# Kernel optimization log

Measured on AMD Instinct MI355X. Metric: run time of the kernel, lower is better.

Reference implementation:

```python
import jax, jax.numpy as jnp
import numpy as np

D_MODEL = 1024
NUM_HEADS = 16
D_K = D_MODEL // NUM_HEADS
EPS = 1e-6


def setup_inputs() -> dict:
    key = jax.random.key(0)
    ks = jax.random.split(key, 16)
    B, S = 2, 2048
    sc_in = 1.0 / np.sqrt(D_MODEL)
    sc_na = 1.0 / np.sqrt(D_K)
    inp = {
        "Q": jax.random.normal(ks[0], (B, S, D_MODEL), jnp.float32),
        "K": jax.random.normal(ks[1], (B, S, D_MODEL), jnp.float32),
        "V": jax.random.normal(ks[2], (B, S, D_MODEL), jnp.float32),
        "mask": jax.random.randint(ks[3], (1, 1, S, S), 0, 2, jnp.int32),
        # projection weights stored [in, out] (math-equivalent to torch Linear)
        "wq": jax.random.normal(ks[4], (D_MODEL, D_MODEL), jnp.float32) * sc_in,
        "bq": jnp.zeros((D_MODEL,), jnp.float32),
        "wk": jax.random.normal(ks[5], (D_MODEL, D_MODEL), jnp.float32) * sc_in,
        "bk": jnp.zeros((D_MODEL,), jnp.float32),
        "wv": jax.random.normal(ks[6], (D_MODEL, D_MODEL), jnp.float32) * sc_in,
        "bv": jnp.zeros((D_MODEL,), jnp.float32),
        "wo": jax.random.normal(ks[7], (D_MODEL, D_MODEL), jnp.float32) * sc_in,
        "bo": jnp.zeros((D_MODEL,), jnp.float32),
        # NeuralAttention score-fn params (per-head-dim transforms)
        "wnq": jax.random.normal(ks[8], (D_K, D_K), jnp.float32) * sc_na,
        "bnq": jnp.zeros((D_K,), jnp.float32),
        "wnk": jax.random.normal(ks[9], (D_K, D_K), jnp.float32) * sc_na,
        "bnk": jnp.zeros((D_K,), jnp.float32),
        "temperature": jnp.ones((NUM_HEADS, 1, 1), jnp.float32),
        "gamma": jnp.ones((D_MODEL,), jnp.float32),
    }
    return inp


def _split_heads(x):
    B, S, _ = x.shape
    return x.reshape(B, S, NUM_HEADS, D_K).transpose(0, 2, 1, 3)  # [B,H,S,dk]


def reference(Q, K, V, mask, wq, bq, wk, bk, wv, bv, wo, bo,
              wnq, bnq, wnk, bnk, temperature, gamma):
    B, S, _ = Q.shape
    q = _split_heads(Q @ wq + bq)  # [B,H,S,dk]
    k = _split_heads(K @ wk + bk)
    v = _split_heads(V @ wv + bv)
    # NeuralAttention: nonlinear per-token feature maps, then contraction
    qf = jnp.tanh(q @ wnq + bnq)
    kf = jnp.tanh(k @ wnk + bnk)
    scores = jnp.einsum('bhqd,bhkd->bhqk', qf, kf) / jnp.sqrt(jnp.float32(D_K))
    scores = scores / temperature  # [H,1,1] broadcasts over [B,H,S,S]
    scores = jnp.where(mask == 0, jnp.float32(-1e9), scores)
    attn = jax.nn.softmax(scores, axis=-1)
    ctx = jnp.einsum('bhqk,bhkd->bhqd', attn, v)
    out = ctx.transpose(0, 2, 1, 3).reshape(B, S, D_MODEL) @ wo + bo
    # RMSNorm
    rms = jax.lax.rsqrt(jnp.mean(out * out, axis=-1, keepdims=True) + EPS)
    return out * rms * gamma
```

## Files before the change

kernel.cpp:

```cpp
#include <hip/hip_runtime.h>
#include <hip/hip_bf16.h>
#include <math.h>

#define S_LEN 2048
#define BATCH 2
#define NH 16
#define DK 64
#define DM 1024
#define BS (BATCH * S_LEN)
#define BHS (BATCH * NH * S_LEN)

using bf16x8  = __attribute__((ext_vector_type(8))) __bf16;
using floatx4 = __attribute__((ext_vector_type(4))) float;
using ushort8v = __attribute__((ext_vector_type(8))) unsigned short;
using ushort4v = __attribute__((ext_vector_type(4))) unsigned short;

__device__ __forceinline__ unsigned short f2bf(float f) {
    union { float f; unsigned u; } v; v.f = f;
    unsigned r = v.u + 0x7fffu + ((v.u >> 16) & 1u);
    return (unsigned short)(r >> 16);
}

__device__ __forceinline__ void gl2lds16(const void* g, void* l) {
    __builtin_amdgcn_global_load_lds(
        (__attribute__((address_space(1))) void*)(uintptr_t)g,
        (__attribute__((address_space(3))) void*)(uintptr_t)l,
        16, 0, 0);
}

__global__ void k_convert(const float* __restrict__ q, const float* __restrict__ k,
                          const float* __restrict__ v,
                          unsigned short* __restrict__ qb, unsigned short* __restrict__ kb,
                          unsigned short* __restrict__ vb) {
    const int N4 = BS * DM / 4;
    int i = blockIdx.x * 256 + threadIdx.x;
    int which = i / N4;
    int off = i - which * N4;
    const floatx4* src = (const floatx4*)(which == 0 ? q : which == 1 ? k : v);
    unsigned short* dst = which == 0 ? qb : which == 1 ? kb : vb;
    floatx4 x = src[off];
    ushort4v o;
    o[0] = f2bf(x[0]); o[1] = f2bf(x[1]); o[2] = f2bf(x[2]); o[3] = f2bf(x[3]);
    ((ushort4v*)dst)[off] = o;
}

__global__ void k_transpose(const float* s0, const float* s1, const float* s2, const float* s3,
                            unsigned short* d0, unsigned short* d1, unsigned short* d2,
                            unsigned short* d3, int n) {
    int z = blockIdx.z;
    const float* src = z == 0 ? s0 : z == 1 ? s1 : z == 2 ? s2 : s3;
    unsigned short* dst = z == 0 ? d0 : z == 1 ? d1 : z == 2 ? d2 : d3;
    __shared__ unsigned short tile[32][33];
    int tx = threadIdx.x & 31, ty = threadIdx.x >> 5;
#pragma unroll
    for (int i = 0; i < 4; i++) {
        int y = blockIdx.y * 32 + i * 8 + ty;
        tile[i * 8 + ty][tx] = f2bf(src[(size_t)y * n + blockIdx.x * 32 + tx]);
    }
    __syncthreads();
#pragma unroll
    for (int i = 0; i < 4; i++) {
        int r = blockIdx.x * 32 + i * 8 + ty;
        dst[(size_t)r * n + blockIdx.y * 32 + tx] = tile[tx][i * 8 + ty];
    }
}

__global__ void k_maskpack(const int* __restrict__ mask, unsigned int* __restrict__ mb) {
    int t = blockIdx.x * 256 + threadIdx.x;
    int row = t >> 6, w = t & 63;
    const int* p = mask + (size_t)row * S_LEN + w * 32;
    unsigned bits = 0;
#pragma unroll
    for (int i = 0; i < 32; i++) bits |= (p[i] != 0 ? 1u : 0u) << i;
    mb[t] = bits;
}

__global__ __launch_bounds__(256) void k_gemm_qkv(
    const unsigned short* __restrict__ Qb, const unsigned short* __restrict__ Kb,
    const unsigned short* __restrict__ Vb,
    const unsigned short* __restrict__ Wqt, const unsigned short* __restrict__ Wkt,
    const unsigned short* __restrict__ Wvt,
    const float* __restrict__ bq, const float* __restrict__ bk, const float* __restrict__ bv,
    unsigned short* __restrict__ qh, unsigned short* __restrict__ kh,
    unsigned short* __restrict__ vfrag) {
    const int K = DM;
    int z = blockIdx.z;
    const unsigned short* A  = z == 0 ? Qb  : z == 1 ? Kb  : Vb;
    const unsigned short* Wt = z == 0 ? Wqt : z == 1 ? Wkt : Wvt;
    const float* bias        = z == 0 ? bq  : z == 1 ? bk  : bv;
    int m0 = blockIdx.y * 128, n0 = blockIdx.x * 128;
    __shared__ unsigned short As[128 * 32];
    __shared__ unsigned short Bs[128 * 32];
    int tid = threadIdx.x;
    int lane = tid & 63, wid = tid >> 6;
    int wy = wid >> 1, wx = wid & 1;
    int l16 = lane & 15, quad = lane >> 4;

    floatx4 acc[4][4] = {};

    for (int kt = 0; kt < K / 32; kt++) {
        int kk = kt * 32;
#pragma unroll
        for (int i = 0; i < 2; i++) {
            int c = i * 256 + tid;
            int row = c >> 2, seg = c & 3;
            gl2lds16(A + (size_t)(m0 + row) * K + kk + seg * 8, &As[c * 8]);
            gl2lds16(Wt + (size_t)(n0 + row) * K + kk + seg * 8, &Bs[c * 8]);
        }
        __syncthreads();
        bf16x8 af[4], bf[4];
#pragma unroll
        for (int mi = 0; mi < 4; mi++)
            af[mi] = *(const bf16x8*)&As[(wy * 64 + mi * 16 + l16) * 32 + quad * 8];
#pragma unroll
        for (int ni = 0; ni < 4; ni++)
            bf[ni] = *(const bf16x8*)&Bs[(wx * 64 + ni * 16 + l16) * 32 + quad * 8];
#pragma unroll
        for (int mi = 0; mi < 4; mi++)
#pragma unroll
            for (int ni = 0; ni < 4; ni++)
                acc[mi][ni] = __builtin_amdgcn_mfma_f32_16x16x32_bf16(af[mi], bf[ni], acc[mi][ni], 0, 0, 0);
        __syncthreads();
    }

#pragma unroll
    for (int mi = 0; mi < 4; mi++) {
#pragma unroll
        for (int ni = 0; ni < 4; ni++) {
            int col = n0 + wx * 64 + ni * 16 + l16;
            float bvv = bias[col];
            int row = m0 + wy * 64 + mi * 16 + quad * 4;
            int b = row >> 11;
            int head = col >> 6;
            int d = col & 63;
            if (z < 2) {
                unsigned short* out = z == 0 ? qh : kh;
                int s = row & (S_LEN - 1);
#pragma unroll
                for (int r = 0; r < 4; r++)
                    out[(size_t)((b * NH + head) * S_LEN + s + r) * DK + d] =
                        f2bf(acc[mi][ni][r] + bvv);
            } else {
                int bh = b * NH + head;
                int kt2 = (row & (S_LEN - 1)) >> 6;
                int ks = mi >> 1;
                int qf = (mi * 2 + (quad >> 1)) & 3;
                int j0 = (quad & 1) * 4;
                size_t off = ((size_t)bh * 32 + kt2) * 4096 +
                             (size_t)(((d >> 4) * 2 + ks) * 512 + (qf * 16 + (d & 15)) * 8 + j0);
                ushort4v o;
#pragma unroll
                for (int r = 0; r < 4; r++) o[r] = f2bf(acc[mi][ni][r] + bvv);
                *(ushort4v*)&vfrag[off] = o;
            }
        }
    }
}

__global__ __launch_bounds__(256) void k_gemm_out(const unsigned short* __restrict__ A,
                                                  const unsigned short* __restrict__ Wt,
                                                  const float* __restrict__ bias,
                                                  float* __restrict__ out_f32) {
    const int K = DM;
    int m0 = blockIdx.y * 128, n0 = blockIdx.x * 128;
    __shared__ unsigned short As[128 * 32];
    __shared__ unsigned short Bs[128 * 32];
    int tid = threadIdx.x;
    int lane = tid & 63, wid = tid >> 6;
    int wy = wid >> 1, wx = wid & 1;
    int l16 = lane & 15, quad = lane >> 4;

    floatx4 acc[4][4] = {};

    for (int kt = 0; kt < K / 32; kt++) {
        int kk = kt * 32;
#pragma unroll
        for (int i = 0; i < 2; i++) {
            int c = i * 256 + tid;
            int row = c >> 2, seg = c & 3;
            gl2lds16(A + (size_t)(m0 + row) * K + kk + seg * 8, &As[c * 8]);
            gl2lds16(Wt + (size_t)(n0 + row) * K + kk + seg * 8, &Bs[c * 8]);
        }
        __syncthreads();
        bf16x8 af[4], bf[4];
#pragma unroll
        for (int mi = 0; mi < 4; mi++)
            af[mi] = *(const bf16x8*)&As[(wy * 64 + mi * 16 + l16) * 32 + quad * 8];
#pragma unroll
        for (int ni = 0; ni < 4; ni++)
            bf[ni] = *(const bf16x8*)&Bs[(wx * 64 + ni * 16 + l16) * 32 + quad * 8];
#pragma unroll
        for (int mi = 0; mi < 4; mi++)
#pragma unroll
            for (int ni = 0; ni < 4; ni++)
                acc[mi][ni] = __builtin_amdgcn_mfma_f32_16x16x32_bf16(af[mi], bf[ni], acc[mi][ni], 0, 0, 0);
        __syncthreads();
    }

#pragma unroll
    for (int mi = 0; mi < 4; mi++) {
#pragma unroll
        for (int ni = 0; ni < 4; ni++) {
            int col = n0 + wx * 64 + ni * 16 + l16;
            float bvv = bias[col];
#pragma unroll
            for (int r = 0; r < 4; r++) {
                int row = m0 + wy * 64 + mi * 16 + quad * 4 + r;
                out_f32[(size_t)row * DM + col] = acc[mi][ni][r] + bvv;
            }
        }
    }
}

__global__ __launch_bounds__(256) void k_feature(const unsigned short* __restrict__ qh,
                                                 const unsigned short* __restrict__ kh,
                                                 const unsigned short* __restrict__ wnqt,
                                                 const unsigned short* __restrict__ wnkt,
                                                 const float* __restrict__ bnq,
                                                 const float* __restrict__ bnk,
                                                 unsigned short* __restrict__ qfb,
                                                 unsigned short* __restrict__ kfrag) {
    int zy = blockIdx.y;
    const unsigned short* src = zy == 0 ? qh : kh;
    const unsigned short* wt = zy == 0 ? wnqt : wnkt;
    const float* bias = zy == 0 ? bnq : bnk;

    int tid = threadIdx.x, lane = tid & 63, wid = tid >> 6;
    int l16 = lane & 15, quad = lane >> 4;
    int r0 = blockIdx.x * 64 + wid * 16;

    bf16x8 af[2];
#pragma unroll
    for (int ks = 0; ks < 2; ks++)
        af[ks] = *(const bf16x8*)(src + (size_t)(r0 + l16) * DK + ks * 32 + quad * 8);

    floatx4 acc[4] = {};
#pragma unroll
    for (int ni = 0; ni < 4; ni++) {
#pragma unroll
        for (int ks = 0; ks < 2; ks++) {
            bf16x8 bf = *(const bf16x8*)(wt + (size_t)(ni * 16 + l16) * DK + ks * 32 + quad * 8);
            acc[ni] = __builtin_amdgcn_mfma_f32_16x16x32_bf16(af[ks], bf, acc[ni], 0, 0, 0);
        }
    }
    if (zy == 0) {
#pragma unroll
        for (int ni = 0; ni < 4; ni++) {
            int col = ni * 16 + l16;
            float bv = bias[col];
#pragma unroll
            for (int r = 0; r < 4; r++) {
                float t = tanhf(acc[ni][r] + bv);
                qfb[(size_t)(r0 + quad * 4 + r) * DK + col] = f2bf(t);
            }
        }
    } else {
        int bh = r0 >> 11;
        int kt = (r0 & (S_LEN - 1)) >> 6;
        size_t base = ((size_t)bh * 32 + kt) * 4096;
#pragma unroll
        for (int ni = 0; ni < 4; ni++) {
            int col = ni * 16 + l16;
            float bv = bias[col];
            int ks = ni >> 1;
            int qf = (ni * 2 + (l16 >> 3)) & 3;
            int j = l16 & 7;
            size_t fo = base + (size_t)((wid * 2 + ks) * 512 + qf * 128 + j);
#pragma unroll
            for (int r = 0; r < 4; r++) {
                float t = tanhf(acc[ni][r] + bv);
                kfrag[fo + (quad * 4 + r) * 8] = f2bf(t);
            }
        }
    }
}

#define PSTR 72
__global__ __launch_bounds__(256, 4) void k_attn(const unsigned short* __restrict__ qf,
                                                 const unsigned short* __restrict__ kfr,
                                                 const unsigned short* __restrict__ vfr,
                                                 const unsigned long long* __restrict__ mb64,
                                                 const float* __restrict__ temp,
                                                 unsigned short* __restrict__ ctx) {
    int tid = threadIdx.x, lane = tid & 63, wid = tid >> 6;
    int l16 = lane & 15, quad = lane >> 4;
    int bh = blockIdx.y;
    int b = bh >> 4, h = bh & 15;
    int q0 = blockIdx.x * 64 + wid * 16;

    const unsigned short* qfb = qf + (size_t)bh * S_LEN * DK;
    const unsigned short* kbase = kfr + (size_t)bh * 32 * 4096;
    const unsigned short* vbase = vfr + (size_t)bh * 32 * 4096;
    float scale = 1.0f / (8.0f * temp[h]);

    __shared__ unsigned short Kbuf[2][4096];
    __shared__ unsigned short Plds[4][16 * PSTR];
    unsigned short* myP = Plds[wid];

    bf16x8 aq[2];
#pragma unroll
    for (int ks = 0; ks < 2; ks++)
        aq[ks] = *(const bf16x8*)(qfb + (size_t)(q0 + l16) * DK + ks * 32 + quad * 8);

    gl2lds16(kbase + tid * 8, &Kbuf[0][tid * 8]);
    gl2lds16(kbase + 2048 + tid * 8, &Kbuf[0][2048 + tid * 8]);

    floatx4 oacc[4] = {};
    float l_part[4] = {0.f, 0.f, 0.f, 0.f};
    int qrow = q0 + quad * 4;

    for (int kt = 0; kt < S_LEN / 64; kt++) {
        __syncthreads();
        int nb = (kt + 1) & 1;
        const unsigned short* kn = kbase + (size_t)((kt + 1) & 31) * 4096;
        gl2lds16(kn + tid * 8, &Kbuf[nb][tid * 8]);
        gl2lds16(kn + 2048 + tid * 8, &Kbuf[nb][2048 + tid * 8]);
        const unsigned short* vt = vbase + (size_t)kt * 4096 + lane * 8;
        bf16x8 vf[8];
#pragma unroll
        for (int i = 0; i < 8; i++) vf[i] = *(const bf16x8*)(vt + i * 512);
        unsigned long long mrow[4];
#pragma unroll
        for (int r = 0; r < 4; r++) mrow[r] = mb64[(size_t)(qrow + r) * 32 + kt];
        const unsigned short* kb = &Kbuf[kt & 1][lane * 8];
        bf16x8 kf8[8];
#pragma unroll
        for (int i = 0; i < 8; i++) kf8[i] = *(const bf16x8*)(kb + i * 512);
        floatx4 sf[4];
#pragma unroll
        for (int ni = 0; ni < 4; ni++) {
            floatx4 z = {};
            z = __builtin_amdgcn_mfma_f32_16x16x32_bf16(aq[0], kf8[ni * 2], z, 0, 0, 0);
            z = __builtin_amdgcn_mfma_f32_16x16x32_bf16(aq[1], kf8[ni * 2 + 1], z, 0, 0, 0);
            sf[ni] = z;
        }
#pragma unroll
        for (int ni = 0; ni < 4; ni++)
#pragma unroll
            for (int r = 0; r < 4; r++) {
                float s = ((mrow[r] >> (ni * 16 + l16)) & 1ull) ? sf[ni][r] * scale : -1e9f;
                float p = __expf(s);
                l_part[r] += p;
                myP[(quad * 4 + r) * PSTR + ni * 16 + l16] = f2bf(p);
            }
        bf16x8 pa[2];
#pragma unroll
        for (int ks = 0; ks < 2; ks++)
            pa[ks] = *(const bf16x8*)&myP[l16 * PSTR + ks * 32 + quad * 8];
#pragma unroll
        for (int ni = 0; ni < 4; ni++) {
            oacc[ni] = __builtin_amdgcn_mfma_f32_16x16x32_bf16(pa[0], vf[ni * 2], oacc[ni], 0, 0, 0);
            oacc[ni] = __builtin_amdgcn_mfma_f32_16x16x32_bf16(pa[1], vf[ni * 2 + 1], oacc[ni], 0, 0, 0);
        }
    }
#pragma unroll
    for (int r = 0; r < 4; r++) {
#pragma unroll
        for (int off = 1; off < 16; off <<= 1)
            l_part[r] += __shfl_xor(l_part[r], off, 16);
    }
    float inv[4];
#pragma unroll
    for (int r = 0; r < 4; r++) inv[r] = 1.0f / l_part[r];
#pragma unroll
    for (int ni = 0; ni < 4; ni++) {
        int d = ni * 16 + l16;
#pragma unroll
        for (int r = 0; r < 4; r++) {
            int s = q0 + quad * 4 + r;
            float val = oacc[ni][r] * inv[r];
            ctx[(size_t)(b * S_LEN + s) * DM + h * DK + d] = f2bf(val);
        }
    }
}

__global__ __launch_bounds__(256) void k_rmsnorm(const float* __restrict__ x,
                                                 const float* __restrict__ gamma,
                                                 float* __restrict__ out) {
    int row = blockIdx.x, tid = threadIdx.x;
    const floatx4* xr = (const floatx4*)(x + (size_t)row * DM);
    floatx4 v = xr[tid];
    float ss = v[0] * v[0] + v[1] * v[1] + v[2] * v[2] + v[3] * v[3];
#pragma unroll
    for (int off = 1; off < 64; off <<= 1) ss += __shfl_xor(ss, off);
    __shared__ float red[4];
    int lane = tid & 63, wid = tid >> 6;
    if (lane == 0) red[wid] = ss;
    __syncthreads();
    float tot = red[0] + red[1] + red[2] + red[3];
    float rms = rsqrtf(tot * (1.0f / DM) + 1e-6f);
    floatx4 g = ((const floatx4*)gamma)[tid];
    floatx4 o;
    o[0] = v[0] * rms * g[0];
    o[1] = v[1] * rms * g[1];
    o[2] = v[2] * rms * g[2];
    o[3] = v[3] * rms * g[3];
    ((floatx4*)(out + (size_t)row * DM))[tid] = o;
}

extern "C" void kernel_launch(void* const* d_in, const int* in_sizes, int n_in,
                              void* d_out, int out_size, void* d_ws, size_t ws_size,
                              hipStream_t stream) {
    const float* Q = (const float*)d_in[0];
    const float* K = (const float*)d_in[1];
    const float* V = (const float*)d_in[2];
    const int* mask = (const int*)d_in[3];
    const float* wq = (const float*)d_in[4];
    const float* bq = (const float*)d_in[5];
    const float* wk = (const float*)d_in[6];
    const float* bk = (const float*)d_in[7];
    const float* wv = (const float*)d_in[8];
    const float* bv = (const float*)d_in[9];
    const float* wo = (const float*)d_in[10];
    const float* bo = (const float*)d_in[11];
    const float* wnq = (const float*)d_in[12];
    const float* bnq = (const float*)d_in[13];
    const float* wnk = (const float*)d_in[14];
    const float* bnk = (const float*)d_in[15];
    const float* temp = (const float*)d_in[16];
    const float* gamma = (const float*)d_in[17];

    char* w = (char*)d_ws;
    size_t o = 0;
    auto alloc = [&](size_t bytes) {
        char* p = w + o;
        o += (bytes + 255) & ~(size_t)255;
        return p;
    };
    unsigned short* Qb = (unsigned short*)alloc((size_t)BS * DM * 2);
    unsigned short* Kb = (unsigned short*)alloc((size_t)BS * DM * 2);
    unsigned short* Vb = (unsigned short*)alloc((size_t)BS * DM * 2);
    unsigned short* Wqt = (unsigned short*)alloc((size_t)DM * DM * 2);
    unsigned short* Wkt = (unsigned short*)alloc((size_t)DM * DM * 2);
    unsigned short* Wvt = (unsigned short*)alloc((size_t)DM * DM * 2);
    unsigned short* Wot = (unsigned short*)alloc((size_t)DM * DM * 2);
    unsigned short* wnqt = (unsigned short*)alloc((size_t)DK * DK * 2);
    unsigned short* wnkt = (unsigned short*)alloc((size_t)DK * DK * 2);
    unsigned short* qh = (unsigned short*)alloc((size_t)BHS * DK * 2);
    unsigned short* kh = (unsigned short*)alloc((size_t)BHS * DK * 2);
    unsigned short* vfrag = (unsigned short*)alloc((size_t)BHS * DK * 2);
    unsigned short* qfb = (unsigned short*)alloc((size_t)BHS * DK * 2);
    unsigned short* kfrag = (unsigned short*)alloc((size_t)BHS * DK * 2);
    unsigned int* mb = (unsigned int*)alloc((size_t)S_LEN * (S_LEN / 32) * 4);
    unsigned short* ctx = (unsigned short*)alloc((size_t)BS * DM * 2);
    float* outt = (float*)alloc((size_t)BS * DM * 4);

    k_convert<<<dim3(3 * BS * DM / 4 / 256), 256, 0, stream>>>(Q, K, V, Qb, Kb, Vb);
    k_transpose<<<dim3(32, 32, 4), 256, 0, stream>>>(wq, wk, wv, wo, Wqt, Wkt, Wvt, Wot, DM);
    k_transpose<<<dim3(2, 2, 2), 256, 0, stream>>>(wnq, wnk, wnq, wnq, wnqt, wnkt, wnqt, wnqt, DK);
    k_maskpack<<<dim3(S_LEN * 64 / 256), 256, 0, stream>>>(mask, mb);

    k_gemm_qkv<<<dim3(8, 32, 3), 256, 0, stream>>>(Qb, Kb, Vb, Wqt, Wkt, Wvt,
                                                   bq, bk, bv, qh, kh, vfrag);

    k_feature<<<dim3(BHS / 64, 2), 256, 0, stream>>>(qh, kh, wnqt, wnkt, bnq, bnk, qfb, kfrag);

    k_attn<<<dim3(S_LEN / 64, BATCH * NH), 256, 0, stream>>>(
        qfb, kfrag, vfrag, (const unsigned long long*)mb, temp, ctx);

    k_gemm_out<<<dim3(8, 32), 256, 0, stream>>>(ctx, Wot, bo, outt);
    k_rmsnorm<<<dim3(BS), 256, 0, stream>>>(outt, gamma, (float*)d_out);
}
```

Baseline: 362.8 us.

## Stage epilogue stores through LDS, fold softmax scale into features, use exp2

Result: faster. 313.3 us (-13.6%).

```diff
diff --git a/kernel.cpp b/kernel.cpp
--- a/kernel.cpp
+++ b/kernel.cpp
@@ -9,16 +9,30 @@
 #define DM 1024
 #define BS (BATCH * S_LEN)
 #define BHS (BATCH * NH * S_LEN)
+#define TRP 72
+#define PSTR 72
 
 using bf16x8  = __attribute__((ext_vector_type(8))) __bf16;
 using floatx4 = __attribute__((ext_vector_type(4))) float;
-using ushort8v = __attribute__((ext_vector_type(8))) unsigned short;
 using ushort4v = __attribute__((ext_vector_type(4))) unsigned short;
+
+extern "C" __device__ float __ocml_exp2_f32(float);
 
 __device__ __forceinline__ unsigned short f2bf(float f) {
     union { float f; unsigned u; } v; v.f = f;
     unsigned r = v.u + 0x7fffu + ((v.u >> 16) & 1u);
     return (unsigned short)(r >> 16);
+}
+
+__device__ __forceinline__ unsigned cvt_pk_bf16(float a, float b) {
+    unsigned r;
+    asm("v_cvt_pk_bf16_f32 %0, %1, %2" : "=v"(r) : "v"(a), "v"(b));
+    return r;
+}
+
+__device__ __forceinline__ float fast_tanh(float x) {
+    float e = __ocml_exp2_f32(x * 2.8853900817779268f);
+    return 1.0f - 2.0f / (e + 1.0f);
 }
 
 __device__ __forceinline__ void gl2lds16(const void* g, void* l) {
@@ -40,7 +54,10 @@
     unsigned short* dst = which == 0 ? qb : which == 1 ? kb : vb;
     floatx4 x = src[off];
     ushort4v o;
-    o[0] = f2bf(x[0]); o[1] = f2bf(x[1]); o[2] = f2bf(x[2]); o[3] = f2bf(x[3]);
+    unsigned p01 = cvt_pk_bf16(x[0], x[1]);
+    unsigned p23 = cvt_pk_bf16(x[2], x[3]);
+    o[0] = (unsigned short)p01; o[1] = (unsigned short)(p01 >> 16);
+    o[2] = (unsigned short)p23; o[3] = (unsigned short)(p23 >> 16);
     ((ushort4v*)dst)[off] = o;
 }
 
@@ -91,6 +108,7 @@
     int m0 = blockIdx.y * 128, n0 = blockIdx.x * 128;
     __shared__ unsigned short As[128 * 32];
     __shared__ unsigned short Bs[128 * 32];
+    __shared__ unsigned short Tr[4][32 * TRP];
     int tid = threadIdx.x;
     int lane = tid & 63, wid = tid >> 6;
     int wy = wid >> 1, wx = wid & 1;
@@ -123,35 +141,66 @@
         __syncthreads();
     }
 
-#pragma unroll
-    for (int mi = 0; mi < 4; mi++) {
-#pragma unroll
-        for (int ni = 0; ni < 4; ni++) {
-            int col = n0 + wx * 64 + ni * 16 + l16;
-            float bvv = bias[col];
-            int row = m0 + wy * 64 + mi * 16 + quad * 4;
-            int b = row >> 11;
-            int head = col >> 6;
-            int d = col & 63;
-            if (z < 2) {
-                unsigned short* out = z == 0 ? qh : kh;
-                int s = row & (S_LEN - 1);
-#pragma unroll
-                for (int r = 0; r < 4; r++)
-                    out[(size_t)((b * NH + head) * S_LEN + s + r) * DK + d] =
-                        f2bf(acc[mi][ni][r] + bvv);
-            } else {
-                int bh = b * NH + head;
-                int kt2 = (row & (S_LEN - 1)) >> 6;
-                int ks = mi >> 1;
-                int qf = (mi * 2 + (quad >> 1)) & 3;
-                int j0 = (quad & 1) * 4;
-                size_t off = ((size_t)bh * 32 + kt2) * 4096 +
-                             (size_t)(((d >> 4) * 2 + ks) * 512 + (qf * 16 + (d & 15)) * 8 + j0);
-                ushort4v o;
-#pragma unroll
-                for (int r = 0; r < 4; r++) o[r] = f2bf(acc[mi][ni][r] + bvv);
-                *(ushort4v*)&vfrag[off] = o;
+    float bvv[4];
+#pragma unroll
+    for (int ni = 0; ni < 4; ni++) bvv[ni] = bias[n0 + wx * 64 + ni * 16 + l16];
+    int head = (n0 + wx * 64) >> 6;
+    int mbase = m0 + wy * 64;
+    int b = mbase >> 11;
+    unsigned short* tw = &Tr[wid][0];
+
+    if (z < 2) {
+        unsigned short* out = z == 0 ? qh : kh;
+        size_t rowbase = (size_t)((b * NH + head) * S_LEN + (mbase & (S_LEN - 1))) * DK;
+#pragma unroll
+        for (int hh = 0; hh < 2; hh++) {
+#pragma unroll
+            for (int mi2 = 0; mi2 < 2; mi2++) {
+                int mi = hh * 2 + mi2;
+#pragma unroll
+                for (int ni = 0; ni < 4; ni++) {
+                    unsigned p01 = cvt_pk_bf16(acc[mi][ni][0] + bvv[ni], acc[mi][ni][1] + bvv[ni]);
+                    unsigned p23 = cvt_pk_bf16(acc[mi][ni][2] + bvv[ni], acc[mi][ni][3] + bvv[ni]);
+                    int ad = (mi2 * 16 + quad * 4) * TRP + ni * 16 + l16;
+                    tw[ad] = (unsigned short)p01;
+                    tw[ad + TRP] = (unsigned short)(p01 >> 16);
+                    tw[ad + 2 * TRP] = (unsigned short)p23;
+                    tw[ad + 3 * TRP] = (unsigned short)(p23 >> 16);
+                }
+            }
+#pragma unroll
+            for (int c = 0; c < 4; c++) {
+                int g = c * 64 + lane;
+                int ml = g >> 3, dc = g & 7;
+                bf16x8 vv = *(const bf16x8*)&tw[ml * TRP + dc * 8];
+                *(bf16x8*)&out[rowbase + (size_t)(hh * 32 + ml) * DK + dc * 8] = vv;
+            }
+        }
+    } else {
+        int kt2 = (mbase & (S_LEN - 1)) >> 6;
+        size_t tilebase = ((size_t)(b * NH + head) * 32 + kt2) * 4096;
+#pragma unroll
+        for (int hh = 0; hh < 2; hh++) {
+#pragma unroll
+            for (int ni2 = 0; ni2 < 2; ni2++) {
+                int ni = hh * 2 + ni2;
+#pragma unroll
+                for (int mi = 0; mi < 4; mi++) {
+                    unsigned p01 = cvt_pk_bf16(acc[mi][ni][0] + bvv[ni], acc[mi][ni][1] + bvv[ni]);
+                    unsigned p23 = cvt_pk_bf16(acc[mi][ni][2] + bvv[ni], acc[mi][ni][3] + bvv[ni]);
+                    int ad = (ni2 * 16 + l16) * TRP + mi * 16 + quad * 4;
+                    *(unsigned*)&tw[ad] = p01;
+                    *(unsigned*)&tw[ad + 2] = p23;
+                }
+            }
+#pragma unroll
+            for (int c = 0; c < 4; c++) {
+                int g = c * 64 + lane;
+                int lt = g & 63;
+                int qt = lt >> 4, l16t = lt & 15;
+                int ad = ((c >> 1) * 16 + l16t) * TRP + (c & 1) * 32 + qt * 8;
+                bf16x8 vv = *(const bf16x8*)&tw[ad];
+                *(bf16x8*)&vfrag[tilebase + (size_t)(4 * hh + c) * 512 + lt * 8] = vv;
             }
         }
     }
@@ -218,6 +267,7 @@
                                                  const unsigned short* __restrict__ wnkt,
                                                  const float* __restrict__ bnq,
                                                  const float* __restrict__ bnk,
+                                                 const float* __restrict__ temp,
                                                  unsigned short* __restrict__ qfb,
                                                  unsigned short* __restrict__ kfrag) {
     int zy = blockIdx.y;
@@ -225,62 +275,70 @@
     const unsigned short* wt = zy == 0 ? wnqt : wnkt;
     const float* bias = zy == 0 ? bnq : bnk;
 
+    __shared__ unsigned short Tr[64 * TRP];
     int tid = threadIdx.x, lane = tid & 63, wid = tid >> 6;
     int l16 = lane & 15, quad = lane >> 4;
-    int r0 = blockIdx.x * 64 + wid * 16;
+    int row0 = blockIdx.x * 64;
+    int bh = row0 >> 11, h = bh & 15;
+    float sc = (zy == 0) ? 1.4426950408889634f / (8.0f * temp[h]) : 1.0f;
 
     bf16x8 af[2];
 #pragma unroll
     for (int ks = 0; ks < 2; ks++)
-        af[ks] = *(const bf16x8*)(src + (size_t)(r0 + l16) * DK + ks * 32 + quad * 8);
+        af[ks] = *(const bf16x8*)(src + (size_t)(row0 + wid * 16 + l16) * DK + ks * 32 + quad * 8);
 
     floatx4 acc[4] = {};
 #pragma unroll
     for (int ni = 0; ni < 4; ni++) {
 #pragma unroll
         for (int ks = 0; ks < 2; ks++) {
-            bf16x8 bf = *(const bf16x8*)(wt + (size_t)(ni * 16 + l16) * DK + ks * 32 + quad * 8);
-            acc[ni] = __builtin_amdgcn_mfma_f32_16x16x32_bf16(af[ks], bf, acc[ni], 0, 0, 0);
-        }
-    }
+            bf16x8 bfr = *(const bf16x8*)(wt + (size_t)(ni * 16 + l16) * DK + ks * 32 + quad * 8);
+            acc[ni] = __builtin_amdgcn_mfma_f32_16x16x32_bf16(af[ks], bfr, acc[ni], 0, 0, 0);
+        }
+    }
+#pragma unroll
+    for (int ni = 0; ni < 4; ni++) {
+        float bv = bias[ni * 16 + l16];
+        float t0 = fast_tanh(acc[ni][0] + bv) * sc;
+        float t1 = fast_tanh(acc[ni][1] + bv) * sc;
+        float t2 = fast_tanh(acc[ni][2] + bv) * sc;
+        float t3 = fast_tanh(acc[ni][3] + bv) * sc;
+        unsigned p01 = cvt_pk_bf16(t0, t1);
+        unsigned p23 = cvt_pk_bf16(t2, t3);
+        int ad = (wid * 16 + quad * 4) * TRP + ni * 16 + l16;
+        Tr[ad] = (unsigned short)p01;
+        Tr[ad + TRP] = (unsigned short)(p01 >> 16);
+        Tr[ad + 2 * TRP] = (unsigned short)p23;
+        Tr[ad + 3 * TRP] = (unsigned short)(p23 >> 16);
+    }
+    __syncthreads();
     if (zy == 0) {
 #pragma unroll
-        for (int ni = 0; ni < 4; ni++) {
-            int col = ni * 16 + l16;
-            float bv = bias[col];
-#pragma unroll
-            for (int r = 0; r < 4; r++) {
-                float t = tanhf(acc[ni][r] + bv);
-                qfb[(size_t)(r0 + quad * 4 + r) * DK + col] = f2bf(t);
-            }
+        for (int c = 0; c < 2; c++) {
+            int g = c * 256 + tid;
+            int ml = g >> 3, dc = g & 7;
+            bf16x8 vv = *(const bf16x8*)&Tr[ml * TRP + dc * 8];
+            *(bf16x8*)&qfb[(size_t)(row0 + ml) * DK + dc * 8] = vv;
         }
     } else {
-        int bh = r0 >> 11;
-        int kt = (r0 & (S_LEN - 1)) >> 6;
-        size_t base = ((size_t)bh * 32 + kt) * 4096;
-#pragma unroll
-        for (int ni = 0; ni < 4; ni++) {
-            int col = ni * 16 + l16;
-            float bv = bias[col];
-            int ks = ni >> 1;
-            int qf = (ni * 2 + (l16 >> 3)) & 3;
-            int j = l16 & 7;
-            size_t fo = base + (size_t)((wid * 2 + ks) * 512 + qf * 128 + j);
-#pragma unroll
-            for (int r = 0; r < 4; r++) {
-                float t = tanhf(acc[ni][r] + bv);
-                kfrag[fo + (quad * 4 + r) * 8] = f2bf(t);
-            }
-        }
-    }
-}
-
-#define PSTR 72
+        int kt = (row0 & (S_LEN - 1)) >> 6;
+        size_t tb = ((size_t)bh * 32 + kt) * 4096;
+#pragma unroll
+        for (int c = 0; c < 2; c++) {
+            int F = c * 256 + tid;
+            int i = F >> 6, lt = F & 63;
+            int qt = lt >> 4, lt16 = lt & 15;
+            int ad = ((i >> 1) * 16 + lt16) * TRP + (i & 1) * 32 + qt * 8;
+            bf16x8 vv = *(const bf16x8*)&Tr[ad];
+            *(bf16x8*)&kfrag[tb + (size_t)i * 512 + lt * 8] = vv;
+        }
+    }
+}
+
 __global__ __launch_bounds__(256, 4) void k_attn(const unsigned short* __restrict__ qf,
                                                  const unsigned short* __restrict__ kfr,
                                                  const unsigned short* __restrict__ vfr,
                                                  const unsigned long long* __restrict__ mb64,
-                                                 const float* __restrict__ temp,
                                                  unsigned short* __restrict__ ctx) {
     int tid = threadIdx.x, lane = tid & 63, wid = tid >> 6;
     int l16 = lane & 15, quad = lane >> 4;
@@ -291,7 +349,6 @@
     const unsigned short* qfb = qf + (size_t)bh * S_LEN * DK;
     const unsigned short* kbase = kfr + (size_t)bh * 32 * 4096;
     const unsigned short* vbase = vfr + (size_t)bh * 32 * 4096;
-    float scale = 1.0f / (8.0f * temp[h]);
 
     __shared__ unsigned short Kbuf[2][4096];
     __shared__ unsigned short Plds[4][16 * PSTR];
@@ -307,7 +364,7 @@
 
     floatx4 oacc[4] = {};
     float l_part[4] = {0.f, 0.f, 0.f, 0.f};
-    int qrow = q0 + quad * 4;
+    const unsigned long long* mrow = mb64 + (size_t)(q0 + quad * 4) * 32;
 
     for (int kt = 0; kt < S_LEN / 64; kt++) {
         __syncthreads();
@@ -319,9 +376,13 @@
         bf16x8 vf[8];
 #pragma unroll
         for (int i = 0; i < 8; i++) vf[i] = *(const bf16x8*)(vt + i * 512);
-        unsigned long long mrow[4];
-#pragma unroll
-        for (int r = 0; r < 4; r++) mrow[r] = mb64[(size_t)(qrow + r) * 32 + kt];
+        unsigned wlo[4], whi[4];
+#pragma unroll
+        for (int r = 0; r < 4; r++) {
+            unsigned long long m = mrow[r * 32 + kt];
+            wlo[r] = (unsigned)(m >> l16);
+            whi[r] = (unsigned)(m >> (l16 + 32));
+        }
         const unsigned short* kb = &Kbuf[kt & 1][lane * 8];
         bf16x8 kf8[8];
 #pragma unroll
@@ -335,14 +396,21 @@
             sf[ni] = z;
         }
 #pragma unroll
-        for (int ni = 0; ni < 4; ni++)
+        for (int ni2 = 0; ni2 < 2; ni2++) {
 #pragma unroll
             for (int r = 0; r < 4; r++) {
-                float s = ((mrow[r] >> (ni * 16 + l16)) & 1ull) ? sf[ni][r] * scale : -1e9f;
-                float p = __expf(s);
-                l_part[r] += p;
-                myP[(quad * 4 + r) * PSTR + ni * 16 + l16] = f2bf(p);
+                unsigned wv = ni2 ? whi[r] : wlo[r];
+                float sA = (wv & 1u) ? sf[2 * ni2][r] : -23.0f;
+                float sB = (wv & 0x10000u) ? sf[2 * ni2 + 1][r] : -23.0f;
+                float pA = __ocml_exp2_f32(sA);
+                float pB = __ocml_exp2_f32(sB);
+                l_part[r] += pA + pB;
+                unsigned pk = cvt_pk_bf16(pA, pB);
+                int ad = (quad * 4 + r) * PSTR + ni2 * 32 + l16;
+                myP[ad] = (unsigned short)pk;
+                myP[ad + 16] = (unsigned short)(pk >> 16);
             }
+        }
         bf16x8 pa[2];
 #pragma unroll
         for (int ks = 0; ks < 2; ks++)
@@ -368,8 +436,7 @@
 #pragma unroll
         for (int r = 0; r < 4; r++) {
             int s = q0 + quad * 4 + r;
-            float val = oacc[ni][r] * inv[r];
-            ctx[(size_t)(b * S_LEN + s) * DM + h * DK + d] = f2bf(val);
+            ctx[(size_t)(b * S_LEN + s) * DM + h * DK + d] = f2bf(oacc[ni][r] * inv[r]);
         }
     }
 }
@@ -453,10 +520,11 @@
     k_gemm_qkv<<<dim3(8, 32, 3), 256, 0, stream>>>(Qb, Kb, Vb, Wqt, Wkt, Wvt,
                                                    bq, bk, bv, qh, kh, vfrag);
 
-    k_feature<<<dim3(BHS / 64, 2), 256, 0, stream>>>(qh, kh, wnqt, wnkt, bnq, bnk, qfb, kfrag);
+    k_feature<<<dim3(BHS / 64, 2), 256, 0, stream>>>(qh, kh, wnqt, wnkt, bnq, bnk, temp,
+                                                     qfb, kfrag);
 
     k_attn<<<dim3(S_LEN / 64, BATCH * NH), 256, 0, stream>>>(
-        qfb, kfrag, vfrag, (const unsigned long long*)mb, temp, ctx);
+        qfb, kfrag, vfrag, (const unsigned long long*)mb, ctx);
 
     k_gemm_out<<<dim3(8, 32), 256, 0, stream>>>(ctx, Wot, bo, outt);
     k_rmsnorm<<<dim3(BS), 256, 0, stream>>>(outt, gamma, (float*)d_out);
```
